# Kernel optimization log

Hardware: AMD Instinct MI355X
Metric: run time of the kernel (lower is better)

Reference implementation:

```python
import jax, jax.numpy as jnp
import numpy as np

N_CLASSES = 1000
FEAT_DIM = 1024
PROJ_DIM = 256
BATCH = 32
NUM_SUPPORT = 8192


def setup_inputs() -> dict:
    key = jax.random.key(0)
    k1, k2, k3, k4 = jax.random.split(key, 4)
    x = jax.random.normal(k1, (BATCH, FEAT_DIM), dtype=jnp.float32)
    sx = jax.random.normal(k2, (NUM_SUPPORT, FEAT_DIM), dtype=jnp.float32)
    # xavier_uniform_ on (1, feat_dim, proj_dim): bound = sqrt(6/(feat+proj))
    bound = float(np.sqrt(6.0 / (FEAT_DIM + PROJ_DIM)))
    proj_weight = jax.random.uniform(k3, (FEAT_DIM, PROJ_DIM), dtype=jnp.float32,
                                     minval=-bound, maxval=bound)
    sy = jax.random.randint(k4, (NUM_SUPPORT,), 0, N_CLASSES, dtype=jnp.int64)
    return {"x": x, "sx": sx, "proj_weight": proj_weight, "sy": sy}


def reference(x, sx, proj_weight, sy):
    # One-hot support labels: (N, C)
    sy_oh = jax.nn.one_hot(sy, N_CLASSES, dtype=jnp.float32)
    # Low-rank projection (shared support set -> project once; identical math
    # to the original's per-batch bmm with a repeated weight).
    xq = x @ proj_weight            # (b, p)
    sxp = sx @ proj_weight          # (N, p)
    # Euclidean kernel: scores = -||xq_i - sxp_j||^2, shape (b, N)
    x_sq = jnp.sum(xq * xq, axis=-1, keepdims=True)       # (b, 1)
    s_sq = jnp.sum(sxp * sxp, axis=-1)[None, :]           # (1, N)
    scores = -(x_sq + s_sq - 2.0 * (xq @ sxp.T))          # (b, N)
    probs = jax.nn.softmax(scores, axis=-1)               # (b, N)
    out = probs @ sy_oh                                   # (b, C)
    return jnp.log(out + 1e-12)
```

## Files before the change

### kernel.cpp

```cpp
#include <hip/hip_runtime.h>
#include <math.h>

#define N_CLASSES 1000
#define FEAT_DIM 1024
#define PROJ_DIM 256
#define BATCH 32
#define NUM_SUPPORT 8192

#define PA_BLOCKS 8192
#define PW_BLOCKS 16
#define PX_BLOCKS 256
#define PZ_BLOCKS 256

typedef __attribute__((ext_vector_type(8))) _Float16 f16x8;
typedef __attribute__((ext_vector_type(4))) _Float16 f16x4;
typedef __attribute__((ext_vector_type(2))) _Float16 f16x2;
typedef __attribute__((ext_vector_type(4))) float f32x4;

__global__ __launch_bounds__(256) void prelude_kernel(
    const float* __restrict__ sx, const float* __restrict__ W,
    const float* __restrict__ x, _Float16* __restrict__ A1,
    _Float16* __restrict__ W1, _Float16* __restrict__ xqh2,
    float* __restrict__ sc) {
  __shared__ float part[256];
  __shared__ _Float16 Lw[256][66];
  const int bid = blockIdx.x;
  const int t = threadIdx.x;

  if (bid < PA_BLOCKS) {
    const int r = bid;
    const float4 v = *(const float4*)&sx[(size_t)r * FEAT_DIM + t * 4];
    f16x4 h = {(_Float16)v.x, (_Float16)v.y, (_Float16)v.z, (_Float16)v.w};
    *(f16x4*)&A1[(size_t)r * FEAT_DIM + t * 4] = h;
  } else if (bid < PA_BLOCKS + PW_BLOCKS) {
    const int k0 = (bid - PA_BLOCKS) * 64;
#pragma unroll 8
    for (int kk = 0; kk < 64; kk++) {
      Lw[t][kk] = (_Float16)W[(size_t)(k0 + kk) * PROJ_DIM + t];
    }
    __syncthreads();
#pragma unroll
    for (int i = 0; i < 8; i++) {
      *(f16x8*)&W1[(size_t)t * FEAT_DIM + k0 + i * 8] = *(f16x8*)&Lw[t][i * 8];
    }
  } else if (bid < PA_BLOCKS + PW_BLOCKS + PX_BLOCKS) {
    const int pxb = bid - PA_BLOCKS - PW_BLOCKS;
    const int b = pxb >> 3, cc = pxb & 7;
    const int col = t & 31, ks = t >> 5;
    const int gc = cc * 32 + col;
    const int k0 = ks * 128;
    float s = 0.f;
#pragma unroll 8
    for (int k = 0; k < 128; k++) {
      s = fmaf(x[(size_t)b * FEAT_DIM + k0 + k],
               W[(size_t)(k0 + k) * PROJ_DIM + gc], s);
    }
    part[t] = s;
    __syncthreads();
    if (t < 32) {
      float acc = 0.f;
#pragma unroll
      for (int i = 0; i < 8; i++) acc += part[i * 32 + t];
      xqh2[(size_t)b * PROJ_DIM + cc * 32 + t] = (_Float16)(2.0f * acc);
    }
  } else {
    const int zb = bid - PA_BLOCKS - PW_BLOCKS - PX_BLOCKS;
    float4 z = {0.f, 0.f, 0.f, 0.f};
    *(float4*)&sc[(size_t)zb * 1024 + t * 4] = z;
  }
}

__global__ __launch_bounds__(256) void gemm_score_kernel(
    const _Float16* __restrict__ A1, const _Float16* __restrict__ W1,
    const _Float16* __restrict__ xqh2, float* __restrict__ sc) {
  __shared__ _Float16 At[64 * 64];
  __shared__ _Float16 Bt[64 * 64];
  __shared__ _Float16 Sx[64 * 72];
  __shared__ _Float16 Xl[32 * 64];

  const int tid = threadIdx.x;
  const int w = tid >> 6;
  const int lane = tid & 63;
  const int xcd = blockIdx.x & 7;
  const int idx = blockIdx.x >> 3;
  const int bm = (xcd * 16 + (idx & 15)) * 64;
  const int bn = (idx >> 4) * 64;
  const int wm = w & 1, wn = w >> 1;
  const int m16 = lane & 15, quad = lane >> 4;
  const int lrow8 = lane >> 3;
  const int g = (lane & 7) ^ lrow8;

  {
    const int r = tid >> 3, c = tid & 7;
    *(f16x8*)&Xl[r * 64 + c * 8] =
        *(const f16x8*)&xqh2[(size_t)r * PROJ_DIM + bn + c * 8];
  }

  f32x4 acc[2][2];
#pragma unroll
  for (int mt = 0; mt < 2; mt++)
#pragma unroll
    for (int nt = 0; nt < 2; nt++) acc[mt][nt] = (f32x4){0.f, 0.f, 0.f, 0.f};

  for (int kb = 0; kb < FEAT_DIM; kb += 64) {
#pragma unroll
    for (int i = 0; i < 2; i++) {
      const int row = w * 16 + i * 8 + lrow8;
      const _Float16* gp = A1 + (size_t)(bm + row) * FEAT_DIM + kb + g * 8;
      __builtin_amdgcn_global_load_lds(
          (const __attribute__((address_space(1))) void*)gp,
          (__attribute__((address_space(3))) void*)(At + (w * 16 + i * 8) * 64),
          16, 0, 0);
    }
#pragma unroll
    for (int i = 0; i < 2; i++) {
      const int nrow = w * 16 + i * 8 + lrow8;
      const _Float16* gp = W1 + (size_t)(bn + nrow) * FEAT_DIM + kb + g * 8;
      __builtin_amdgcn_global_load_lds(
          (const __attribute__((address_space(1))) void*)gp,
          (__attribute__((address_space(3))) void*)(Bt + (w * 16 + i * 8) * 64),
          16, 0, 0);
    }
    __syncthreads();

#pragma unroll
    for (int s = 0; s < 2; s++) {
      const int slot = (s * 4 + quad) ^ (m16 & 7);
      f16x8 af[2], bf[2];
#pragma unroll
      for (int mt = 0; mt < 2; mt++) {
        const int row = wm * 32 + mt * 16 + m16;
        af[mt] = *(f16x8*)&At[row * 64 + slot * 8];
      }
#pragma unroll
      for (int nt = 0; nt < 2; nt++) {
        const int nrow = wn * 32 + nt * 16 + m16;
        bf[nt] = *(f16x8*)&Bt[nrow * 64 + slot * 8];
      }
#pragma unroll
      for (int mt = 0; mt < 2; mt++)
#pragma unroll
        for (int nt = 0; nt < 2; nt++)
          acc[mt][nt] = __builtin_amdgcn_mfma_f32_16x16x32_f16(
              af[mt], bf[nt], acc[mt][nt], 0, 0, 0);
    }
    __syncthreads();
  }

#pragma unroll
  for (int mt = 0; mt < 2; mt++)
#pragma unroll
    for (int nt = 0; nt < 2; nt++)
#pragma unroll
      for (int r = 0; r < 4; r++) {
        const int jl = wm * 32 + mt * 16 + quad * 4 + r;
        const int nl = wn * 32 + nt * 16 + m16;
        Sx[jl * 72 + nl] = (_Float16)acc[mt][nt][r];
      }
  __syncthreads();

  const int j = tid & 63;
  const int bg = tid >> 6;
  float dotb[8] = {0.f, 0.f, 0.f, 0.f, 0.f, 0.f, 0.f, 0.f};
  float rsq = 0.f;
#pragma unroll
  for (int c = 0; c < 8; c++) {
    const f16x8 hv = *(const f16x8*)&Sx[j * 72 + c * 8];
    const f16x2* hp = (const f16x2*)&hv;
#pragma unroll
    for (int i = 0; i < 4; i++)
      rsq = __builtin_amdgcn_fdot2(hp[i], hp[i], rsq, false);
#pragma unroll
    for (int b8 = 0; b8 < 8; b8++) {
      const f16x8 xv = *(const f16x8*)&Xl[(bg * 8 + b8) * 64 + c * 8];
      const f16x2* xp = (const f16x2*)&xv;
#pragma unroll
      for (int i = 0; i < 4; i++)
        dotb[b8] = __builtin_amdgcn_fdot2(hp[i], xp[i], dotb[b8], false);
    }
  }
#pragma unroll
  for (int b8 = 0; b8 < 8; b8++) {
    atomicAdd(&sc[(size_t)(bg * 8 + b8) * NUM_SUPPORT + bm + j],
              dotb[b8] - rsq);
  }
}

__global__ __launch_bounds__(1024) void finish_kernel(
    const float* __restrict__ sc, const int* __restrict__ sy,
    float* __restrict__ out) {
  __shared__ float cls[N_CLASSES];
  __shared__ float redm[16];
  __shared__ float reds[16];

  const int b = blockIdx.x;
  const int t = threadIdx.x;
  const int lane = t & 63, wave = t >> 6;

  float v[8];
  float m = -1e30f;
#pragma unroll
  for (int jj = 0; jj < 8; jj++) {
    v[jj] = sc[(size_t)b * NUM_SUPPORT + jj * 1024 + t];
    m = fmaxf(m, v[jj]);
  }
#pragma unroll
  for (int o = 1; o < 64; o <<= 1) m = fmaxf(m, __shfl_xor(m, o, 64));
  if (lane == 0) redm[wave] = m;
  if (t < N_CLASSES) cls[t] = 0.0f;
  __syncthreads();
  float gm = redm[0];
#pragma unroll
  for (int i = 1; i < 16; i++) gm = fmaxf(gm, redm[i]);

  float lsum = 0.0f;
#pragma unroll
  for (int jj = 0; jj < 8; jj++) {
    const float e = expf(v[jj] - gm);
    lsum += e;
    atomicAdd(&cls[sy[jj * 1024 + t]], e);
  }
#pragma unroll
  for (int o = 1; o < 64; o <<= 1) lsum += __shfl_xor(lsum, o, 64);
  if (lane == 0) reds[wave] = lsum;
  __syncthreads();
  float total = 0.f;
#pragma unroll
  for (int i = 0; i < 16; i++) total += reds[i];
  const float inv = 1.0f / total;
  if (t < N_CLASSES) {
    out[(size_t)b * N_CLASSES + t] = logf(cls[t] * inv + 1e-12f);
  }
}

extern "C" void kernel_launch(void* const* d_in, const int* in_sizes, int n_in,
                              void* d_out, int out_size, void* d_ws,
                              size_t ws_size, hipStream_t stream) {
  const float* x = (const float*)d_in[0];
  const float* sx = (const float*)d_in[1];
  const float* W = (const float*)d_in[2];
  const int* sy = (const int*)d_in[3];
  float* out = (float*)d_out;

  char* p = (char*)d_ws;
  float* sc = (float*)p;          p += (size_t)BATCH * NUM_SUPPORT * 4;
  _Float16* A1 = (_Float16*)p;    p += (size_t)NUM_SUPPORT * FEAT_DIM * 2;
  _Float16* W1 = (_Float16*)p;    p += (size_t)PROJ_DIM * FEAT_DIM * 2;
  _Float16* xqh2 = (_Float16*)p;

  prelude_kernel<<<dim3(PA_BLOCKS + PW_BLOCKS + PX_BLOCKS + PZ_BLOCKS),
                   dim3(256), 0, stream>>>(sx, W, x, A1, W1, xqh2, sc);
  gemm_score_kernel<<<dim3(512), dim3(256), 0, stream>>>(A1, W1, xqh2, sc);
  finish_kernel<<<dim3(BATCH), dim3(1024), 0, stream>>>(sc, sy, out);
}
```

Before: 120.3 us.

## Fuse sx fp16 conversion into GEMM load and finish into last blocks

Drops the separate prelude pass that converts sx to fp16 in a workspace. The GEMM now loads fp32 sx directly, converts it in registers and writes swizzled fp16 into LDS. The finish kernel is folded into the GEMM kernel through an atomic ticket counter, so the last 32 blocks each spin until every block has finished and then compute one batch row's softmax and class scatter. This removes an extra global round trip of the 16MB sx copy and one launch. The cost is synchronous fp32 loads in place of async global_load_lds, a spin-wait that assumes all blocks are co-resident, and a finish phase run by 256 threads instead of 1024.

```diff
diff --git a/kernel.cpp b/kernel.cpp
--- a/kernel.cpp
+++ b/kernel.cpp
@@ -6,34 +6,27 @@
 #define PROJ_DIM 256
 #define BATCH 32
 #define NUM_SUPPORT 8192
-
-#define PA_BLOCKS 8192
+#define NBLK 512
+
 #define PW_BLOCKS 16
 #define PX_BLOCKS 256
 #define PZ_BLOCKS 256
 
 typedef __attribute__((ext_vector_type(8))) _Float16 f16x8;
-typedef __attribute__((ext_vector_type(4))) _Float16 f16x4;
 typedef __attribute__((ext_vector_type(2))) _Float16 f16x2;
 typedef __attribute__((ext_vector_type(4))) float f32x4;
 
 __global__ __launch_bounds__(256) void prelude_kernel(
-    const float* __restrict__ sx, const float* __restrict__ W,
-    const float* __restrict__ x, _Float16* __restrict__ A1,
+    const float* __restrict__ W, const float* __restrict__ x,
     _Float16* __restrict__ W1, _Float16* __restrict__ xqh2,
-    float* __restrict__ sc) {
+    float* __restrict__ sc, int* __restrict__ counter) {
   __shared__ float part[256];
   __shared__ _Float16 Lw[256][66];
   const int bid = blockIdx.x;
   const int t = threadIdx.x;
 
-  if (bid < PA_BLOCKS) {
-    const int r = bid;
-    const float4 v = *(const float4*)&sx[(size_t)r * FEAT_DIM + t * 4];
-    f16x4 h = {(_Float16)v.x, (_Float16)v.y, (_Float16)v.z, (_Float16)v.w};
-    *(f16x4*)&A1[(size_t)r * FEAT_DIM + t * 4] = h;
-  } else if (bid < PA_BLOCKS + PW_BLOCKS) {
-    const int k0 = (bid - PA_BLOCKS) * 64;
+  if (bid < PW_BLOCKS) {
+    const int k0 = bid * 64;
 #pragma unroll 8
     for (int kk = 0; kk < 64; kk++) {
       Lw[t][kk] = (_Float16)W[(size_t)(k0 + kk) * PROJ_DIM + t];
@@ -43,8 +36,8 @@
     for (int i = 0; i < 8; i++) {
       *(f16x8*)&W1[(size_t)t * FEAT_DIM + k0 + i * 8] = *(f16x8*)&Lw[t][i * 8];
     }
-  } else if (bid < PA_BLOCKS + PW_BLOCKS + PX_BLOCKS) {
-    const int pxb = bid - PA_BLOCKS - PW_BLOCKS;
+  } else if (bid < PW_BLOCKS + PX_BLOCKS) {
+    const int pxb = bid - PW_BLOCKS;
     const int b = pxb >> 3, cc = pxb & 7;
     const int col = t & 31, ks = t >> 5;
     const int gc = cc * 32 + col;
@@ -64,19 +57,25 @@
       xqh2[(size_t)b * PROJ_DIM + cc * 32 + t] = (_Float16)(2.0f * acc);
     }
   } else {
-    const int zb = bid - PA_BLOCKS - PW_BLOCKS - PX_BLOCKS;
+    const int zb = bid - PW_BLOCKS - PX_BLOCKS;
+    if (zb == 0 && t == 0) *counter = 0;
     float4 z = {0.f, 0.f, 0.f, 0.f};
     *(float4*)&sc[(size_t)zb * 1024 + t * 4] = z;
   }
 }
 
-__global__ __launch_bounds__(256) void gemm_score_kernel(
-    const _Float16* __restrict__ A1, const _Float16* __restrict__ W1,
-    const _Float16* __restrict__ xqh2, float* __restrict__ sc) {
+__global__ __launch_bounds__(256) void gemm_score_finish_kernel(
+    const float* __restrict__ sx, const _Float16* __restrict__ W1,
+    const _Float16* __restrict__ xqh2, float* __restrict__ sc,
+    int* __restrict__ counter, const int* __restrict__ sy,
+    float* __restrict__ out) {
   __shared__ _Float16 At[64 * 64];
   __shared__ _Float16 Bt[64 * 64];
   __shared__ _Float16 Sx[64 * 72];
   __shared__ _Float16 Xl[32 * 64];
+  __shared__ float red1[4];
+  __shared__ float red2[4];
+  __shared__ int ticket_s;
 
   const int tid = threadIdx.x;
   const int w = tid >> 6;
@@ -88,7 +87,7 @@
   const int wm = w & 1, wn = w >> 1;
   const int m16 = lane & 15, quad = lane >> 4;
   const int lrow8 = lane >> 3;
-  const int g = (lane & 7) ^ lrow8;
+  const int gB = (lane & 7) ^ lrow8;
 
   {
     const int r = tid >> 3, c = tid & 7;
@@ -96,6 +95,13 @@
         *(const f16x8*)&xqh2[(size_t)r * PROJ_DIM + bn + c * 8];
   }
 
+  const int arow = w * 16 + (lane >> 2);
+  const int cg0 = (lane & 3) * 2;
+  const float* __restrict__ abase =
+      sx + (size_t)(bm + arow) * FEAT_DIM + cg0 * 8;
+  _Float16* __restrict__ ad0 = &At[arow * 64 + ((cg0) ^ (arow & 7)) * 8];
+  _Float16* __restrict__ ad1 = &At[arow * 64 + ((cg0 + 1) ^ (arow & 7)) * 8];
+
   f32x4 acc[2][2];
 #pragma unroll
   for (int mt = 0; mt < 2; mt++)
@@ -103,19 +109,22 @@
     for (int nt = 0; nt < 2; nt++) acc[mt][nt] = (f32x4){0.f, 0.f, 0.f, 0.f};
 
   for (int kb = 0; kb < FEAT_DIM; kb += 64) {
-#pragma unroll
-    for (int i = 0; i < 2; i++) {
-      const int row = w * 16 + i * 8 + lrow8;
-      const _Float16* gp = A1 + (size_t)(bm + row) * FEAT_DIM + kb + g * 8;
-      __builtin_amdgcn_global_load_lds(
-          (const __attribute__((address_space(1))) void*)gp,
-          (__attribute__((address_space(3))) void*)(At + (w * 16 + i * 8) * 64),
-          16, 0, 0);
+    {
+      const float4* gp = (const float4*)(abase + kb);
+      const float4 v0 = gp[0], v1 = gp[1], v2 = gp[2], v3 = gp[3];
+      f16x8 h0 = {(_Float16)v0.x, (_Float16)v0.y, (_Float16)v0.z,
+                  (_Float16)v0.w, (_Float16)v1.x, (_Float16)v1.y,
+                  (_Float16)v1.z, (_Float16)v1.w};
+      f16x8 h1 = {(_Float16)v2.x, (_Float16)v2.y, (_Float16)v2.z,
+                  (_Float16)v2.w, (_Float16)v3.x, (_Float16)v3.y,
+                  (_Float16)v3.z, (_Float16)v3.w};
+      *(f16x8*)ad0 = h0;
+      *(f16x8*)ad1 = h1;
     }
 #pragma unroll
     for (int i = 0; i < 2; i++) {
       const int nrow = w * 16 + i * 8 + lrow8;
-      const _Float16* gp = W1 + (size_t)(bn + nrow) * FEAT_DIM + kb + g * 8;
+      const _Float16* gp = W1 + (size_t)(bn + nrow) * FEAT_DIM + kb + gB * 8;
       __builtin_amdgcn_global_load_lds(
           (const __attribute__((address_space(1))) void*)gp,
           (__attribute__((address_space(3))) void*)(Bt + (w * 16 + i * 8) * 64),
@@ -184,52 +193,54 @@
     atomicAdd(&sc[(size_t)(bg * 8 + b8) * NUM_SUPPORT + bm + j],
               dotb[b8] - rsq);
   }
-}
-
-__global__ __launch_bounds__(1024) void finish_kernel(
-    const float* __restrict__ sc, const int* __restrict__ sy,
-    float* __restrict__ out) {
-  __shared__ float cls[N_CLASSES];
-  __shared__ float redm[16];
-  __shared__ float reds[16];
-
-  const int b = blockIdx.x;
-  const int t = threadIdx.x;
-  const int lane = t & 63, wave = t >> 6;
-
-  float v[8];
+
+  __threadfence();
+  __syncthreads();
+  if (tid == 0) ticket_s = atomicAdd(counter, 1);
+  __syncthreads();
+  const int tk = ticket_s;
+  if (tk < NBLK - BATCH) return;
+
+  const int b = tk - (NBLK - BATCH);
+  if (tid == 0) {
+    while (__hip_atomic_load(counter, __ATOMIC_ACQUIRE,
+                             __HIP_MEMORY_SCOPE_AGENT) < NBLK) {
+    }
+  }
+  __syncthreads();
+  __threadfence();
+
+  float* cls = (float*)At;
+  for (int c = tid; c < N_CLASSES; c += 256) cls[c] = 0.0f;
+
+  float v[32];
   float m = -1e30f;
 #pragma unroll
-  for (int jj = 0; jj < 8; jj++) {
-    v[jj] = sc[(size_t)b * NUM_SUPPORT + jj * 1024 + t];
+  for (int jj = 0; jj < 32; jj++) {
+    v[jj] = sc[(size_t)b * NUM_SUPPORT + jj * 256 + tid];
     m = fmaxf(m, v[jj]);
   }
 #pragma unroll
   for (int o = 1; o < 64; o <<= 1) m = fmaxf(m, __shfl_xor(m, o, 64));
-  if (lane == 0) redm[wave] = m;
-  if (t < N_CLASSES) cls[t] = 0.0f;
-  __syncthreads();
-  float gm = redm[0];
-#pragma unroll
-  for (int i = 1; i < 16; i++) gm = fmaxf(gm, redm[i]);
+  if (lane == 0) red1[w] = m;
+  __syncthreads();
+  const float gm = fmaxf(fmaxf(red1[0], red1[1]), fmaxf(red1[2], red1[3]));
 
   float lsum = 0.0f;
 #pragma unroll
-  for (int jj = 0; jj < 8; jj++) {
+  for (int jj = 0; jj < 32; jj++) {
     const float e = expf(v[jj] - gm);
     lsum += e;
-    atomicAdd(&cls[sy[jj * 1024 + t]], e);
+    atomicAdd(&cls[sy[jj * 256 + tid]], e);
   }
 #pragma unroll
   for (int o = 1; o < 64; o <<= 1) lsum += __shfl_xor(lsum, o, 64);
-  if (lane == 0) reds[wave] = lsum;
-  __syncthreads();
-  float total = 0.f;
-#pragma unroll
-  for (int i = 0; i < 16; i++) total += reds[i];
+  if (lane == 0) red2[w] = lsum;
+  __syncthreads();
+  const float total = (red2[0] + red2[1]) + (red2[2] + red2[3]);
   const float inv = 1.0f / total;
-  if (t < N_CLASSES) {
-    out[(size_t)b * N_CLASSES + t] = logf(cls[t] * inv + 1e-12f);
+  for (int c = tid; c < N_CLASSES; c += 256) {
+    out[(size_t)b * N_CLASSES + c] = logf(cls[c] * inv + 1e-12f);
   }
 }
 
@@ -244,12 +255,12 @@
 
   char* p = (char*)d_ws;
   float* sc = (float*)p;          p += (size_t)BATCH * NUM_SUPPORT * 4;
-  _Float16* A1 = (_Float16*)p;    p += (size_t)NUM_SUPPORT * FEAT_DIM * 2;
   _Float16* W1 = (_Float16*)p;    p += (size_t)PROJ_DIM * FEAT_DIM * 2;
-  _Float16* xqh2 = (_Float16*)p;
-
-  prelude_kernel<<<dim3(PA_BLOCKS + PW_BLOCKS + PX_BLOCKS + PZ_BLOCKS),
-                   dim3(256), 0, stream>>>(sx, W, x, A1, W1, xqh2, sc);
-  gemm_score_kernel<<<dim3(512), dim3(256), 0, stream>>>(A1, W1, xqh2, sc);
-  finish_kernel<<<dim3(BATCH), dim3(1024), 0, stream>>>(sc, sy, out);
+  _Float16* xqh2 = (_Float16*)p;  p += (size_t)BATCH * PROJ_DIM * 2;
+  int* counter = (int*)p;
+
+  prelude_kernel<<<dim3(PW_BLOCKS + PX_BLOCKS + PZ_BLOCKS), dim3(256), 0,
+                   stream>>>(W, x, W1, xqh2, sc, counter);
+  gemm_score_finish_kernel<<<dim3(NBLK), dim3(256), 0, stream>>>(
+      sx, W1, xqh2, sc, counter, sy, out);
 }
```

New measurement: 146.3 us. +21.6%, slower.

## Fuse fp32-to-fp16 conversion of support set into GEMM tile loads

Applied to the files above, without the earlier changes.

Removes the prelude pass that converted the whole support matrix to an fp16 workspace copy. The GEMM kernel now loads fp32 rows directly, converts them in registers and stores them swizzled into LDS. This cuts a large write and re-read of the intermediate buffer, but replaces the asynchronous global-to-LDS loads with synchronous register loads of twice the bytes per tile, repeated across column blocks.

```diff
diff --git a/kernel.cpp b/kernel.cpp
--- a/kernel.cpp
+++ b/kernel.cpp
@@ -7,19 +7,16 @@
 #define BATCH 32
 #define NUM_SUPPORT 8192
 
-#define PA_BLOCKS 8192
 #define PW_BLOCKS 16
 #define PX_BLOCKS 256
 #define PZ_BLOCKS 256
 
 typedef __attribute__((ext_vector_type(8))) _Float16 f16x8;
-typedef __attribute__((ext_vector_type(4))) _Float16 f16x4;
 typedef __attribute__((ext_vector_type(2))) _Float16 f16x2;
 typedef __attribute__((ext_vector_type(4))) float f32x4;
 
 __global__ __launch_bounds__(256) void prelude_kernel(
-    const float* __restrict__ sx, const float* __restrict__ W,
-    const float* __restrict__ x, _Float16* __restrict__ A1,
+    const float* __restrict__ W, const float* __restrict__ x,
     _Float16* __restrict__ W1, _Float16* __restrict__ xqh2,
     float* __restrict__ sc) {
   __shared__ float part[256];
@@ -27,13 +24,8 @@
   const int bid = blockIdx.x;
   const int t = threadIdx.x;
 
-  if (bid < PA_BLOCKS) {
-    const int r = bid;
-    const float4 v = *(const float4*)&sx[(size_t)r * FEAT_DIM + t * 4];
-    f16x4 h = {(_Float16)v.x, (_Float16)v.y, (_Float16)v.z, (_Float16)v.w};
-    *(f16x4*)&A1[(size_t)r * FEAT_DIM + t * 4] = h;
-  } else if (bid < PA_BLOCKS + PW_BLOCKS) {
-    const int k0 = (bid - PA_BLOCKS) * 64;
+  if (bid < PW_BLOCKS) {
+    const int k0 = bid * 64;
 #pragma unroll 8
     for (int kk = 0; kk < 64; kk++) {
       Lw[t][kk] = (_Float16)W[(size_t)(k0 + kk) * PROJ_DIM + t];
@@ -43,8 +35,8 @@
     for (int i = 0; i < 8; i++) {
       *(f16x8*)&W1[(size_t)t * FEAT_DIM + k0 + i * 8] = *(f16x8*)&Lw[t][i * 8];
     }
-  } else if (bid < PA_BLOCKS + PW_BLOCKS + PX_BLOCKS) {
-    const int pxb = bid - PA_BLOCKS - PW_BLOCKS;
+  } else if (bid < PW_BLOCKS + PX_BLOCKS) {
+    const int pxb = bid - PW_BLOCKS;
     const int b = pxb >> 3, cc = pxb & 7;
     const int col = t & 31, ks = t >> 5;
     const int gc = cc * 32 + col;
@@ -64,14 +56,14 @@
       xqh2[(size_t)b * PROJ_DIM + cc * 32 + t] = (_Float16)(2.0f * acc);
     }
   } else {
-    const int zb = bid - PA_BLOCKS - PW_BLOCKS - PX_BLOCKS;
+    const int zb = bid - PW_BLOCKS - PX_BLOCKS;
     float4 z = {0.f, 0.f, 0.f, 0.f};
     *(float4*)&sc[(size_t)zb * 1024 + t * 4] = z;
   }
 }
 
 __global__ __launch_bounds__(256) void gemm_score_kernel(
-    const _Float16* __restrict__ A1, const _Float16* __restrict__ W1,
+    const float* __restrict__ sx, const _Float16* __restrict__ W1,
     const _Float16* __restrict__ xqh2, float* __restrict__ sc) {
   __shared__ _Float16 At[64 * 64];
   __shared__ _Float16 Bt[64 * 64];
@@ -88,7 +80,7 @@
   const int wm = w & 1, wn = w >> 1;
   const int m16 = lane & 15, quad = lane >> 4;
   const int lrow8 = lane >> 3;
-  const int g = (lane & 7) ^ lrow8;
+  const int gB = (lane & 7) ^ lrow8;
 
   {
     const int r = tid >> 3, c = tid & 7;
@@ -96,6 +88,13 @@
         *(const f16x8*)&xqh2[(size_t)r * PROJ_DIM + bn + c * 8];
   }
 
+  const int arow = w * 16 + (lane >> 2);
+  const int cg0 = (lane & 3) * 2;
+  const float* __restrict__ abase =
+      sx + (size_t)(bm + arow) * FEAT_DIM + cg0 * 8;
+  _Float16* __restrict__ ad0 = &At[arow * 64 + ((cg0) ^ (arow & 7)) * 8];
+  _Float16* __restrict__ ad1 = &At[arow * 64 + ((cg0 + 1) ^ (arow & 7)) * 8];
+
   f32x4 acc[2][2];
 #pragma unroll
   for (int mt = 0; mt < 2; mt++)
@@ -103,19 +102,22 @@
     for (int nt = 0; nt < 2; nt++) acc[mt][nt] = (f32x4){0.f, 0.f, 0.f, 0.f};
 
   for (int kb = 0; kb < FEAT_DIM; kb += 64) {
-#pragma unroll
-    for (int i = 0; i < 2; i++) {
-      const int row = w * 16 + i * 8 + lrow8;
-      const _Float16* gp = A1 + (size_t)(bm + row) * FEAT_DIM + kb + g * 8;
-      __builtin_amdgcn_global_load_lds(
-          (const __attribute__((address_space(1))) void*)gp,
-          (__attribute__((address_space(3))) void*)(At + (w * 16 + i * 8) * 64),
-          16, 0, 0);
+    {
+      const float4* gp = (const float4*)(abase + kb);
+      const float4 v0 = gp[0], v1 = gp[1], v2 = gp[2], v3 = gp[3];
+      f16x8 h0 = {(_Float16)v0.x, (_Float16)v0.y, (_Float16)v0.z,
+                  (_Float16)v0.w, (_Float16)v1.x, (_Float16)v1.y,
+                  (_Float16)v1.z, (_Float16)v1.w};
+      f16x8 h1 = {(_Float16)v2.x, (_Float16)v2.y, (_Float16)v2.z,
+                  (_Float16)v2.w, (_Float16)v3.x, (_Float16)v3.y,
+                  (_Float16)v3.z, (_Float16)v3.w};
+      *(f16x8*)ad0 = h0;
+      *(f16x8*)ad1 = h1;
     }
 #pragma unroll
     for (int i = 0; i < 2; i++) {
       const int nrow = w * 16 + i * 8 + lrow8;
-      const _Float16* gp = W1 + (size_t)(bn + nrow) * FEAT_DIM + kb + g * 8;
+      const _Float16* gp = W1 + (size_t)(bn + nrow) * FEAT_DIM + kb + gB * 8;
       __builtin_amdgcn_global_load_lds(
           (const __attribute__((address_space(1))) void*)gp,
           (__attribute__((address_space(3))) void*)(Bt + (w * 16 + i * 8) * 64),
@@ -244,12 +246,11 @@
 
   char* p = (char*)d_ws;
   float* sc = (float*)p;          p += (size_t)BATCH * NUM_SUPPORT * 4;
-  _Float16* A1 = (_Float16*)p;    p += (size_t)NUM_SUPPORT * FEAT_DIM * 2;
   _Float16* W1 = (_Float16*)p;    p += (size_t)PROJ_DIM * FEAT_DIM * 2;
   _Float16* xqh2 = (_Float16*)p;
 
-  prelude_kernel<<<dim3(PA_BLOCKS + PW_BLOCKS + PX_BLOCKS + PZ_BLOCKS),
-                   dim3(256), 0, stream>>>(sx, W, x, A1, W1, xqh2, sc);
-  gemm_score_kernel<<<dim3(512), dim3(256), 0, stream>>>(A1, W1, xqh2, sc);
+  prelude_kernel<<<dim3(PW_BLOCKS + PX_BLOCKS + PZ_BLOCKS), dim3(256), 0,
+                   stream>>>(W, x, W1, xqh2, sc);
+  gemm_score_kernel<<<dim3(512), dim3(256), 0, stream>>>(sx, W1, xqh2, sc);
   finish_kernel<<<dim3(BATCH), dim3(1024), 0, stream>>>(sc, sy, out);
 }
```

After: 114.9 us. 1.05x faster.
